# Kernel tuning notes

Measured on AMD Instinct MI355X. Metric: run time of the kernel, lower is better.

The kernel has to match this reference:

```python
import jax, jax.numpy as jnp
import numpy as np

S, B, D, F, E, K = 1024, 2, 512, 2048, 8, 2


def setup_inputs() -> dict:
    key = jax.random.key(0)
    ks = jax.random.split(key, 12)
    s = lambda *sh: 1.0 / np.sqrt(sh[0])
    inp = {
        "x": jax.random.normal(ks[0], (S, B, D), dtype=jnp.float32),
        # gate: nn.Linear(d_model, n_experts)
        "Wg": jax.random.normal(ks[1], (D, E), dtype=jnp.float32) * s(D),
        "bg": jnp.zeros((E,), dtype=jnp.float32),
        # routed experts: stacked FFN params (E copies of expert)
        "W1": jax.random.normal(ks[2], (E, D, F), dtype=jnp.float32) * s(D),
        "b1": jnp.zeros((E, F), dtype=jnp.float32),
        "W2": jax.random.normal(ks[3], (E, F, D), dtype=jnp.float32) * s(F),
        "b2": jnp.zeros((E, D), dtype=jnp.float32),
        # shared expert (single FFN)
        "Ws1": jax.random.normal(ks[4], (D, F), dtype=jnp.float32) * s(D),
        "bs1": jnp.zeros((F,), dtype=jnp.float32),
        "Ws2": jax.random.normal(ks[5], (F, D), dtype=jnp.float32) * s(F),
        "bs2": jnp.zeros((D,), dtype=jnp.float32),
    }
    return inp


def reference(x, Wg, bg, W1, b1, W2, b2, Ws1, bs1, Ws2, bs2):
    # gate_logits: (S, B, E)
    gate_logits = jnp.einsum("sbd,de->sbe", x, Wg) + bg
    # top-k per token (eval mode: k = n_experts_per_token, t = 1.0)
    weights, selected = jax.lax.top_k(gate_logits, K)  # (S,B,K)
    weights = jax.nn.softmax(weights.astype(jnp.float32), axis=-1)
    # combine weights per expert: (S,B,E)
    onehot = jax.nn.one_hot(selected, E, dtype=weights.dtype)  # (S,B,K,E)
    comb = jnp.einsum("sbk,sbke->sbe", weights, onehot)
    # routed experts computed densely, combined with per-token routing weight
    h = jax.nn.relu(jnp.einsum("sbd,edf->sbef", x, W1) + b1)  # (S,B,E,F)
    y = jnp.einsum("sbef,efd->sbed", h, W2) + b2              # (S,B,E,D)
    out = jnp.einsum("sbe,sbed->sbd", comb, y)
    # shared expert, scaled by 1/k
    hs = jax.nn.relu(jnp.einsum("sbd,df->sbf", x, Ws1) + bs1)
    shared = jnp.einsum("sbf,fd->sbd", hs, Ws2) + bs2
    out = out + (1.0 / K) * shared
    return out
```

## Files before the change

kernel.cpp:

```cpp
#include <hip/hip_runtime.h>
#include <hip/hip_bf16.h>
#include <stdint.h>

#define TT 2048
#define DD 512
#define FF 2048
#define EE 8

typedef unsigned short u16;
typedef __attribute__((ext_vector_type(8))) unsigned short ushort8v;
typedef __attribute__((ext_vector_type(8))) short short8;
typedef __attribute__((ext_vector_type(4))) float float4v;

__device__ __forceinline__ u16 f2bf(float f) {
    unsigned u = __float_as_uint(f);
    u += 0x7FFF + ((u >> 16) & 1);
    return (u16)(u >> 16);
}

__device__ __forceinline__ void gl_lds16(const u16* g, u16* l) {
    __builtin_amdgcn_global_load_lds(
        (const __attribute__((address_space(1))) unsigned int*)g,
        (__attribute__((address_space(3))) unsigned int*)l, 16, 0, 0);
}

#define WS_HB   0ull
#define WS_XG   (WS_HB + 6144ull*2048*2)
#define WS_WT1  (WS_XG + 2048ull*512*2)
#define WS_ME   (WS_WT1 + 9ull*2048*512*2)
#define WS_MW   (WS_ME + 16384)
#define WS_RT   (WS_MW + 16384)
#define WS_WROW (WS_RT + 16384)
#define WS_TROW (WS_WROW + 16384)
#define WS_RTG  (WS_TROW + 16384)
#define WS_WT2  (WS_RTG + 128)
#define WS_YB   (WS_WT2 + 9ull*2048*512*2)
#define YS      (6144ull*512)
#define WS_NEED (WS_YB + 2ull*6144*512*4)

__device__ __forceinline__ void conv_unit(int j, const float* __restrict__ srcE,
                                          const float* __restrict__ srcS,
                                          u16* __restrict__ dst,
                                          int R, int C, int shC, u16* Ls) {
    int mid = j >> 8, t2 = j & 255;
    int tr = t2 >> shC, tc = t2 & ((1 << shC) - 1);
    int r0 = tr * 64, c0 = tc * 64;
    const float* src = (mid < 8) ? srcE + (size_t)mid * R * C : srcS;
    u16* dstm = dst + (size_t)mid * R * C;
    int t = threadIdx.x;
#pragma unroll
    for (int i = 0; i < 4; ++i) {
        int rr = (t >> 4) + i * 16;
        int cc = (t & 15) * 4;
        float4v v = *(const float4v*)(src + (size_t)(r0 + rr) * C + c0 + cc);
#pragma unroll
        for (int jx = 0; jx < 4; ++jx) Ls[(cc + jx) * 72 + rr] = f2bf(v[jx]);
    }
    __syncthreads();
#pragma unroll
    for (int jj = 0; jj < 2; ++jj) {
        int slot = t + jj * 256;
        int cc = slot >> 3, r8 = (slot & 7) * 8;
        ushort8v o = *(const ushort8v*)&Ls[cc * 72 + r8];
        *(ushort8v*)(dstm + (size_t)(c0 + cc) * R + r0 + r8) = o;
    }
}

__device__ __forceinline__ void gate_wave(int t, int lane,
                                          const float* __restrict__ x,
                                          const float* __restrict__ Wg,
                                          const float* __restrict__ bg,
                                          int* __restrict__ metaE,
                                          float* __restrict__ metaW,
                                          u16* __restrict__ xg) {
    const float* xp = x + (size_t)t * DD + lane * 8;
    float4v x0 = *(const float4v*)xp;
    float4v x1 = *(const float4v*)(xp + 4);
    float xf[8] = {x0[0], x0[1], x0[2], x0[3], x1[0], x1[1], x1[2], x1[3]};
    float acc[EE] = {0.f, 0.f, 0.f, 0.f, 0.f, 0.f, 0.f, 0.f};
#pragma unroll
    for (int g = 0; g < 8; ++g) {
        const float* wp = Wg + (size_t)(lane * 8 + g) * EE;
        float4v w0 = *(const float4v*)wp;
        float4v w1 = *(const float4v*)(wp + 4);
        acc[0] += xf[g] * w0[0]; acc[1] += xf[g] * w0[1];
        acc[2] += xf[g] * w0[2]; acc[3] += xf[g] * w0[3];
        acc[4] += xf[g] * w1[0]; acc[5] += xf[g] * w1[1];
        acc[6] += xf[g] * w1[2]; acc[7] += xf[g] * w1[3];
    }
#pragma unroll
    for (int off = 1; off < 64; off <<= 1) {
#pragma unroll
        for (int e = 0; e < EE; ++e) acc[e] += __shfl_xor(acc[e], off, 64);
    }
    ushort8v xv;
#pragma unroll
    for (int jx = 0; jx < 4; ++jx) xv[jx] = f2bf(x0[jx]);
#pragma unroll
    for (int jx = 0; jx < 4; ++jx) xv[4 + jx] = f2bf(x1[jx]);
    *(ushort8v*)(xg + (size_t)t * DD + lane * 8) = xv;
    if (lane == 0) {
#pragma unroll
        for (int e = 0; e < EE; ++e) acc[e] += bg[e];
        int e0 = 0; float l0 = acc[0];
#pragma unroll
        for (int e = 1; e < EE; ++e) if (acc[e] > l0) { l0 = acc[e]; e0 = e; }
        int e1 = -1; float l1 = -3.4e38f;
#pragma unroll
        for (int e = 0; e < EE; ++e)
            if (e != e0 && acc[e] > l1) { l1 = acc[e]; e1 = e; }
        float ex = __expf(l1 - l0);
        float w0 = 1.f / (1.f + ex);
        metaE[2 * t] = e0; metaE[2 * t + 1] = e1;
        metaW[2 * t] = w0; metaW[2 * t + 1] = 1.f - w0;
    }
}

__global__ __launch_bounds__(256) void fused1_k(
    const float* __restrict__ x, const float* __restrict__ Wg,
    const float* __restrict__ bg,
    const float* __restrict__ W1, const float* __restrict__ Ws1,
    const float* __restrict__ W2, const float* __restrict__ Ws2,
    float* __restrict__ out, u16* __restrict__ xg,
    u16* __restrict__ Wt1, u16* __restrict__ Wt2,
    int* __restrict__ metaE, float* __restrict__ metaW, int nconv) {
    __shared__ __align__(16) u16 Ls[64 * 72];
    int b = blockIdx.x, tid = threadIdx.x;
    if (b < nconv) {
        if (b < 2304) conv_unit(b, W1, Ws1, Wt1, DD, FF, 5, Ls);
        else          conv_unit(b - 2304, W2, Ws2, Wt2, FF, DD, 3, Ls);
    } else if (b < nconv + 512) {
        int gb = b - nconv;
        gate_wave(gb * 4 + (tid >> 6), tid & 63, x, Wg, bg, metaE, metaW, xg);
    } else {
        int zb = b - nconv - 512;
        float* op = out + (size_t)zb * 8192;
#pragma unroll
        for (int it = 0; it < 8; ++it)
            *(float4v*)(op + it * 1024 + tid * 4) = (float4v){0.f, 0.f, 0.f, 0.f};
    }
}

__global__ __launch_bounds__(256) void conv2_k(const float* __restrict__ W2,
                                               const float* __restrict__ Ws2,
                                               u16* __restrict__ Wt2) {
    __shared__ __align__(16) u16 Ls[64 * 72];
    conv_unit(blockIdx.x, W2, Ws2, Wt2, FF, DD, 3, Ls);
}

__global__ __launch_bounds__(256) void rank_k(const int* __restrict__ metaE,
                                              const float* __restrict__ metaW,
                                              int* __restrict__ routing,
                                              int* __restrict__ rtok,
                                              float* __restrict__ wrow,
                                              int* __restrict__ trow) {
    __shared__ __align__(16) char smem[16384];
    u16* er      = (u16*)smem;
    int* segCnt  = (int*)(smem + 8192);
    int* segBase = (int*)(smem + 10240);
    int* expTot  = (int*)(smem + 12288);
    int tid = threadIdx.x, wv = tid >> 6, lane = tid & 63;
    unsigned long long below = (lane == 0) ? 0ull : ((~0ull) >> (64 - lane));
    for (int s = wv * 16; s < wv * 16 + 16; ++s) {
        int entry = s * 64 + lane;
        int e = metaE[entry];
        int rk = 0;
#pragma unroll
        for (int ee = 0; ee < 8; ++ee) {
            unsigned long long m = __ballot(e == ee);
            if (e == ee) rk = __popcll(m & below);
            if (lane == ee) segCnt[s * 8 + ee] = __popcll(m);
        }
        er[entry] = (u16)(e | (rk << 4));
    }
    __syncthreads();
    if (tid < 8) {
        int s = 0;
        for (int g = 0; g < 64; ++g) { segBase[g * 8 + tid] = s; s += segCnt[g * 8 + tid]; }
        expTot[tid] = s;
    }
    __syncthreads();
    if (tid == 0) {
        int s = 0;
        for (int e = 0; e < 8; ++e) { int c = expTot[e]; expTot[8 + e] = s; s += c; }
    }
    __syncthreads();
    if (tid < 8) { routing[tid] = expTot[8 + tid]; routing[8 + tid] = expTot[tid]; }
    for (int i = 0; i < 16; ++i) {
        int entry = tid + i * 256;
        int v = er[entry];
        int e = v & 15, rk = v >> 4;
        int row = expTot[8 + e] + segBase[(entry >> 6) * 8 + e] + rk;
        rtok[row] = entry >> 1;
        wrow[row] = metaW[entry];
        trow[entry] = row;
    }
}

__global__ __launch_bounds__(512) void gemmA_k(
    const u16* __restrict__ xg, const u16* __restrict__ Wt1,
    const float* __restrict__ b1, const float* __restrict__ bs1,
    const int* __restrict__ routing, const int* __restrict__ rtok,
    u16* __restrict__ hbuf) {
    __shared__ __align__(16) u16 SM[32768];
    u16* Asb[2] = {SM, SM + 8192};
    u16* Bsb[2] = {SM + 16384, SM + 24576};
    const int* offs = routing; const int* cnt = routing + 8;
    int j = blockIdx.x, tid = threadIdx.x;
    int rt, ct, Mloc, hRowBase, rowBase; bool routed;
    const u16* Bsrc; const float* bias;
    if (j < 256) {
        rt = j >> 4; ct = j & 15; Mloc = 128; rowBase = rt * 128;
        Bsrc = Wt1 + (size_t)8 * FF * DD; bias = bs1;
        hRowBase = 4096 + rt * 128; routed = false;
    } else {
        int jr = j - 256; int e = jr & 7; int rc = jr >> 3;
        rt = rc >> 4; ct = rc & 15;
        int M = cnt[e]; if (rt * 128 >= M) return;
        Mloc = M - rt * 128; if (Mloc > 128) Mloc = 128;
        rowBase = offs[e] + rt * 128;
        Bsrc = Wt1 + (size_t)e * FF * DD; bias = b1 + e * FF;
        hRowBase = rowBase; routed = true;
    }
    int n0 = ct * 128;
    int lane = tid & 63, w = tid >> 6, ln = lane & 15, quad = lane >> 4;
    int wm = w >> 2, wn = w & 3;
    int lr8 = lane >> 3;
    int cs = (lane & 7) ^ lr8;
    const u16* ApS[2];
#pragma unroll
    for (int i = 0; i < 2; ++i) {
        int r = w * 16 + i * 8 + lr8;
        int tok;
        if (routed) { int br = rowBase + r; if (br > 4095) br = 4095; tok = rtok[br]; }
        else tok = rowBase + r;
        ApS[i] = xg + (size_t)tok * DD + cs * 8;
    }
    const u16* BpS[2];
#pragma unroll
    for (int i = 0; i < 2; ++i) {
        int r = w * 16 + i * 8 + lr8;
        BpS[i] = Bsrc + (size_t)(n0 + r) * DD + cs * 8;
    }
    float4v acc[4][2];
#pragma unroll
    for (int a = 0; a < 4; ++a)
#pragma unroll
        for (int b = 0; b < 2; ++b) acc[a][b] = (float4v){0.f, 0.f, 0.f, 0.f};

    auto stage = [&](int kt, int pb) {
#pragma unroll
        for (int i = 0; i < 2; ++i)
            gl_lds16(ApS[i] + kt * 64, Asb[pb] + (w * 16 + i * 8) * 64);
#pragma unroll
        for (int i = 0; i < 2; ++i)
            gl_lds16(BpS[i] + kt * 64, Bsb[pb] + (w * 16 + i * 8) * 64);
    };

    stage(0, 0);
#pragma unroll
    for (int kt = 0; kt < 8; ++kt) {
        int pb = kt & 1;
        if (kt < 7) {
            stage(kt + 1, pb ^ 1);
            asm volatile("s_waitcnt vmcnt(4)" ::: "memory");
        } else {
            asm volatile("s_waitcnt vmcnt(0)" ::: "memory");
        }
        __builtin_amdgcn_s_barrier();
        __builtin_amdgcn_sched_barrier(0);
        const u16* Ab = Asb[pb]; const u16* Bb = Bsb[pb];
#pragma unroll
        for (int s = 0; s < 2; ++s) {
            int chs = ((s * 4 + quad) ^ (ln & 7)) * 8;
            short8 Af[4], Bf[2];
#pragma unroll
            for (int a = 0; a < 4; ++a) {
                int ra = wm * 64 + a * 16 + ln;
                Af[a] = *(const short8*)(Ab + ra * 64 + chs);
            }
#pragma unroll
            for (int b = 0; b < 2; ++b) {
                int rb = wn * 32 + b * 16 + ln;
                Bf[b] = *(const short8*)(Bb + rb * 64 + chs);
            }
#pragma unroll
            for (int a = 0; a < 4; ++a)
#pragma unroll
                for (int b = 0; b < 2; ++b)
                    acc[a][b] = __builtin_amdgcn_mfma_f32_16x16x32_bf16(Af[a], Bf[b], acc[a][b], 0, 0, 0);
        }
        __builtin_amdgcn_sched_barrier(0);
        __builtin_amdgcn_s_barrier();
    }
    __syncthreads();
    u16* Cs = SM;
#pragma unroll
    for (int b = 0; b < 2; ++b) {
        int n = wn * 32 + b * 16 + ln;
        float bv = bias[n0 + n];
#pragma unroll
        for (int a = 0; a < 4; ++a) {
#pragma unroll
            for (int i = 0; i < 4; ++i) {
                int lr = wm * 64 + a * 16 + quad * 4 + i;
                float v = acc[a][b][i] + bv;
                v = v > 0.f ? v : 0.f;
                Cs[lr * 136 + n] = f2bf(v);
            }
        }
    }
    __syncthreads();
#pragma unroll
    for (int p = 0; p < 4; ++p) {
        int idx = p * 512 + tid;
        int row = idx >> 4, ch = idx & 15;
        if (row < Mloc) {
            ushort8v o = *(const ushort8v*)(Cs + row * 136 + ch * 8);
            *(ushort8v*)(hbuf + (size_t)(hRowBase + row) * FF + n0 + ch * 8) = o;
        }
    }
}

__global__ __launch_bounds__(512) void gemmB_k(
    const u16* __restrict__ hbuf, const u16* __restrict__ Wt2,
    const float* __restrict__ b2, const float* __restrict__ bs2,
    const int* __restrict__ routing, float* __restrict__ ybuf) {
    __shared__ __align__(16) u16 As[2][128 * 64];
    __shared__ __align__(16) u16 Bs[2][128 * 64];
    const int* offs = routing; const int* cnt = routing + 8;
    int j = blockIdx.x, tid = threadIdx.x;
    int rt, ct, ks, Mloc, aRowBase;
    const u16* Bsrc; const float* bias;
    if (j < 128) {
        ks = j & 1; ct = (j >> 1) & 3; rt = j >> 3;
        Mloc = 128; aRowBase = 4096 + rt * 128;
        Bsrc = Wt2 + (size_t)8 * DD * FF; bias = bs2;
    } else {
        int jr = j - 128; int e = jr & 7; int rc = jr >> 3;
        ks = rc & 1; ct = (rc >> 1) & 3; rt = rc >> 3;
        int M = cnt[e]; if (rt * 128 >= M) return;
        Mloc = M - rt * 128; if (Mloc > 128) Mloc = 128;
        aRowBase = offs[e] + rt * 128;
        Bsrc = Wt2 + (size_t)e * DD * FF; bias = b2 + e * DD;
    }
    int n0 = ct * 128;
    int lane = tid & 63, w = tid >> 6, ln = lane & 15, quad = lane >> 4;
    int wm = w >> 2, wn = w & 3;
    int lr8 = lane >> 3;
    int cs = (lane & 7) ^ lr8;
    const u16* ApS[2];
#pragma unroll
    for (int i = 0; i < 2; ++i) {
        int r = w * 16 + i * 8 + lr8;
        ApS[i] = hbuf + (size_t)(aRowBase + r) * FF + ks * 1024 + cs * 8;
    }
    const u16* BpS[2];
#pragma unroll
    for (int i = 0; i < 2; ++i) {
        int r = w * 16 + i * 8 + lr8;
        BpS[i] = Bsrc + (size_t)(n0 + r) * FF + ks * 1024 + cs * 8;
    }
    float4v acc[4][2];
#pragma unroll
    for (int a = 0; a < 4; ++a)
#pragma unroll
        for (int b = 0; b < 2; ++b) acc[a][b] = (float4v){0.f, 0.f, 0.f, 0.f};

    auto stage = [&](int kt, int pb) {
#pragma unroll
        for (int i = 0; i < 2; ++i)
            gl_lds16(ApS[i] + kt * 64, &As[pb][0] + (w * 16 + i * 8) * 64);
#pragma unroll
        for (int i = 0; i < 2; ++i)
            gl_lds16(BpS[i] + kt * 64, &Bs[pb][0] + (w * 16 + i * 8) * 64);
    };

    stage(0, 0);
#pragma unroll
    for (int kt = 0; kt < 16; ++kt) {
        int pb = kt & 1;
        if (kt < 15) {
            stage(kt + 1, pb ^ 1);
            asm volatile("s_waitcnt vmcnt(4)" ::: "memory");
        } else {
            asm volatile("s_waitcnt vmcnt(0)" ::: "memory");
        }
        __builtin_amdgcn_s_barrier();
        __builtin_amdgcn_sched_barrier(0);
        const u16* Ab = &As[pb][0]; const u16* Bb = &Bs[pb][0];
#pragma unroll
        for (int s = 0; s < 2; ++s) {
            int chs = ((s * 4 + quad) ^ (ln & 7)) * 8;
            short8 Af[4], Bf[2];
#pragma unroll
            for (int a = 0; a < 4; ++a) {
                int ra = wm * 64 + a * 16 + ln;
                Af[a] = *(const short8*)(Ab + ra * 64 + chs);
            }
#pragma unroll
            for (int b = 0; b < 2; ++b) {
                int rb = wn * 32 + b * 16 + ln;
                Bf[b] = *(const short8*)(Bb + rb * 64 + chs);
            }
#pragma unroll
            for (int a = 0; a < 4; ++a)
#pragma unroll
                for (int b = 0; b < 2; ++b)
                    acc[a][b] = __builtin_amdgcn_mfma_f32_16x16x32_bf16(Af[a], Bf[b], acc[a][b], 0, 0, 0);
        }
        __builtin_amdgcn_sched_barrier(0);
        __builtin_amdgcn_s_barrier();
    }
    float* yb = ybuf + (size_t)ks * YS;
#pragma unroll
    for (int b = 0; b < 2; ++b) {
        int n = n0 + wn * 32 + b * 16 + ln;
        float bv = (ks == 0) ? bias[n] : 0.f;
#pragma unroll
        for (int a = 0; a < 4; ++a) {
#pragma unroll
            for (int i = 0; i < 4; ++i) {
                int lr = wm * 64 + a * 16 + quad * 4 + i;
                if (lr < Mloc)
                    yb[(size_t)(aRowBase + lr) * DD + n] = acc[a][b][i] + bv;
            }
        }
    }
}

__global__ __launch_bounds__(256) void combine_k(
    const float* __restrict__ ybuf, const int* __restrict__ trow,
    const float* __restrict__ metaW, float* __restrict__ out) {
    int tid = threadIdx.x;
    int tok = blockIdx.x * 2 + (tid >> 7);
    int q = (tid & 127) * 4;
    int r0 = trow[2 * tok], r1 = trow[2 * tok + 1];
    float w0 = metaW[2 * tok], w1 = metaW[2 * tok + 1];
    const float* ya = ybuf;
    const float* yb = ybuf + YS;
    float4v y0a = *(const float4v*)(ya + (size_t)r0 * DD + q);
    float4v y0b = *(const float4v*)(yb + (size_t)r0 * DD + q);
    float4v y1a = *(const float4v*)(ya + (size_t)r1 * DD + q);
    float4v y1b = *(const float4v*)(yb + (size_t)r1 * DD + q);
    float4v ysa = *(const float4v*)(ya + (size_t)(4096 + tok) * DD + q);
    float4v ysb = *(const float4v*)(yb + (size_t)(4096 + tok) * DD + q);
    float4v o;
#pragma unroll
    for (int i = 0; i < 4; ++i)
        o[i] = w0 * (y0a[i] + y0b[i]) + w1 * (y1a[i] + y1b[i]) + 0.5f * (ysa[i] + ysb[i]);
    *(float4v*)(out + (size_t)tok * DD + q) = o;
}

__global__ __launch_bounds__(256) void gemmBat_k(
    const u16* __restrict__ hbuf, const u16* __restrict__ Wt2,
    const float* __restrict__ b2, const float* __restrict__ bs2,
    const int* __restrict__ routing, const int* __restrict__ rtok,
    const float* __restrict__ wrow, float* __restrict__ out) {
    __shared__ __align__(16) u16 As[2][64 * 64];
    __shared__ __align__(16) u16 Bs[2][128 * 64];
    const int* offs = routing; const int* cnt = routing + 8;
    int j = blockIdx.x, tid = threadIdx.x;
    int rt, ct, ks, Mloc, aRowBase; bool sh;
    const u16* Bsrc; const float* bias;
    if (j < 256) {
        sh = true; rt = j >> 3; int sub = j & 7; ct = sub >> 1; ks = sub & 1;
        Mloc = 64; aRowBase = 4096 + rt * 64;
        Bsrc = Wt2 + (size_t)8 * DD * FF; bias = bs2;
    } else {
        sh = false; int jr = j - 256; int e = jr & 7; int rc = jr >> 3;
        rt = rc >> 3; ct = (rc >> 1) & 3; ks = rc & 1;
        int M = cnt[e]; if (rt * 64 >= M) return;
        Mloc = M - rt * 64; if (Mloc > 64) Mloc = 64;
        aRowBase = offs[e] + rt * 64;
        Bsrc = Wt2 + (size_t)e * DD * FF; bias = b2 + e * DD;
    }
    int n0 = ct * 128;
    int lane = tid & 63, w = tid >> 6, ln = lane & 15, quad = lane >> 4;
    int lr8 = lane >> 3;
    int cs = (lane & 7) ^ lr8;
    const u16* ApS[2];
#pragma unroll
    for (int i = 0; i < 2; ++i) {
        int r = w * 16 + i * 8 + lr8;
        ApS[i] = hbuf + (size_t)(aRowBase + r) * FF + ks * 1024 + cs * 8;
    }
    const u16* BpS[4];
#pragma unroll
    for (int i = 0; i < 4; ++i) {
        int r = w * 32 + i * 8 + lr8;
        BpS[i] = Bsrc + (size_t)(n0 + r) * FF + ks * 1024 + cs * 8;
    }
    float4v acc[2][4];
#pragma unroll
    for (int a = 0; a < 2; ++a)
#pragma unroll
        for (int b = 0; b < 4; ++b) acc[a][b] = (float4v){0.f, 0.f, 0.f, 0.f};
    auto stage = [&](int kt, int pb) {
        u16* Ab = &As[pb][0]; u16* Bb = &Bs[pb][0];
#pragma unroll
        for (int i = 0; i < 2; ++i)
            gl_lds16(ApS[i] + kt * 64, Ab + (w * 16 + i * 8) * 64);
#pragma unroll
        for (int i = 0; i < 4; ++i)
            gl_lds16(BpS[i] + kt * 64, Bb + (w * 32 + i * 8) * 64);
    };
    stage(0, 0);
#pragma unroll
    for (int kt = 0; kt < 16; ++kt) {
        int pb = kt & 1;
        if (kt < 15) {
            stage(kt + 1, pb ^ 1);
            asm volatile("s_waitcnt vmcnt(6)" ::: "memory");
        } else {
            asm volatile("s_waitcnt vmcnt(0)" ::: "memory");
        }
        __builtin_amdgcn_s_barrier();
        __builtin_amdgcn_sched_barrier(0);
        const u16* Ab = &As[pb][0]; const u16* Bb = &Bs[pb][0];
#pragma unroll
        for (int s = 0; s < 2; ++s) {
            int chs = ((s * 4 + quad) ^ (ln & 7)) * 8;
            short8 Af[2], Bf[4];
#pragma unroll
            for (int a = 0; a < 2; ++a) {
                int ra = (w & 1) * 32 + a * 16 + ln;
                Af[a] = *(const short8*)(Ab + ra * 64 + chs);
            }
#pragma unroll
            for (int b = 0; b < 4; ++b) {
                int rb = (w >> 1) * 64 + b * 16 + ln;
                Bf[b] = *(const short8*)(Bb + rb * 64 + chs);
            }
#pragma unroll
            for (int a = 0; a < 2; ++a)
#pragma unroll
                for (int b = 0; b < 4; ++b)
                    acc[a][b] = __builtin_amdgcn_mfma_f32_16x16x32_bf16(Af[a], Bf[b], acc[a][b], 0, 0, 0);
        }
        __builtin_amdgcn_sched_barrier(0);
        __builtin_amdgcn_s_barrier();
    }
    float bv[4];
#pragma unroll
    for (int b = 0; b < 4; ++b)
        bv[b] = (ks == 0) ? bias[n0 + (w >> 1) * 64 + b * 16 + ln] : 0.f;
#pragma unroll
    for (int a = 0; a < 2; ++a) {
#pragma unroll
        for (int i = 0; i < 4; ++i) {
            int lr = (w & 1) * 32 + a * 16 + quad * 4 + i;
            if (lr < Mloc) {
                int row = aRowBase + lr;
                int t; float wr;
                if (sh) { t = row - 4096; wr = 0.5f; }
                else    { t = rtok[row]; wr = wrow[row]; }
                float* op = out + (size_t)t * DD;
#pragma unroll
                for (int b = 0; b < 4; ++b) {
                    int n = n0 + (w >> 1) * 64 + b * 16 + ln;
                    atomicAdd(op + n, wr * (acc[a][b][i] + bv[b]));
                }
            }
        }
    }
}

extern "C" void kernel_launch(void* const* d_in, const int* in_sizes, int n_in,
                              void* d_out, int out_size, void* d_ws, size_t ws_size,
                              hipStream_t stream) {
    const float* x   = (const float*)d_in[0];
    const float* Wg  = (const float*)d_in[1];
    const float* bg  = (const float*)d_in[2];
    const float* W1  = (const float*)d_in[3];
    const float* b1  = (const float*)d_in[4];
    const float* W2  = (const float*)d_in[5];
    const float* b2  = (const float*)d_in[6];
    const float* Ws1 = (const float*)d_in[7];
    const float* bs1 = (const float*)d_in[8];
    const float* Ws2 = (const float*)d_in[9];
    const float* bs2 = (const float*)d_in[10];
    float* out = (float*)d_out;

    char* ws = (char*)d_ws;
    u16*   hbuf    = (u16*)(ws + WS_HB);
    u16*   xg      = (u16*)(ws + WS_XG);
    u16*   Wt1     = (u16*)(ws + WS_WT1);
    int*   metaE   = (int*)(ws + WS_ME);
    float* metaW   = (float*)(ws + WS_MW);
    int*   rtok    = (int*)(ws + WS_RT);
    float* wrow    = (float*)(ws + WS_WROW);
    int*   trow    = (int*)(ws + WS_TROW);
    int*   routing = (int*)(ws + WS_RTG);
    bool   big     = ws_size >= WS_NEED;
    u16*   Wt2     = big ? (u16*)(ws + WS_WT2) : Wt1;
    float* ybuf    = (float*)(ws + WS_YB);
    int    nconv   = big ? 4608 : 2304;
    int    ngrid1  = big ? (nconv + 512) : (nconv + 640);

    fused1_k<<<ngrid1, 256, 0, stream>>>(x, Wg, bg, W1, Ws1, W2, Ws2,
                                         out, xg, Wt1, Wt2, metaE, metaW, nconv);
    rank_k<<<1, 256, 0, stream>>>(metaE, metaW, routing, rtok, wrow, trow);
    gemmA_k<<<4352, 512, 0, stream>>>(xg, Wt1, b1, bs1, routing, rtok, hbuf);
    if (big) {
        gemmB_k<<<2176, 512, 0, stream>>>(hbuf, Wt2, b2, bs2, routing, ybuf);
        combine_k<<<1024, 256, 0, stream>>>(ybuf, trow, metaW, out);
    } else {
        conv2_k<<<2304, 256, 0, stream>>>(W2, Ws2, Wt2);
        gemmBat_k<<<4352, 256, 0, stream>>>(hbuf, Wt2, b2, bs2, routing, rtok, wrow, out);
    }
}
```

Baseline: 196.8 us.

## Drop split-K in second expert GEMM and swizzle LDS in weight conversion

```diff
diff --git a/kernel.cpp b/kernel.cpp
--- a/kernel.cpp
+++ b/kernel.cpp
@@ -54,14 +54,19 @@
         int cc = (t & 15) * 4;
         float4v v = *(const float4v*)(src + (size_t)(r0 + rr) * C + c0 + cc);
 #pragma unroll
-        for (int jx = 0; jx < 4; ++jx) Ls[(cc + jx) * 72 + rr] = f2bf(v[jx]);
+        for (int jx = 0; jx < 4; ++jx) {
+            int c = cc + jx;
+            int rs = rr ^ (((c >> 2) & 3) << 4);
+            Ls[c * 72 + rs] = f2bf(v[jx]);
+        }
     }
     __syncthreads();
 #pragma unroll
     for (int jj = 0; jj < 2; ++jj) {
         int slot = t + jj * 256;
         int cc = slot >> 3, r8 = (slot & 7) * 8;
-        ushort8v o = *(const ushort8v*)&Ls[cc * 72 + r8];
+        int r8s = r8 ^ (((cc >> 2) & 3) << 4);
+        ushort8v o = *(const ushort8v*)&Ls[cc * 72 + r8s];
         *(ushort8v*)(dstm + (size_t)(c0 + cc) * R + r0 + r8) = o;
     }
 }
@@ -330,15 +335,15 @@
     __shared__ __align__(16) u16 Bs[2][128 * 64];
     const int* offs = routing; const int* cnt = routing + 8;
     int j = blockIdx.x, tid = threadIdx.x;
-    int rt, ct, ks, Mloc, aRowBase;
+    int rt, ct, Mloc, aRowBase;
     const u16* Bsrc; const float* bias;
-    if (j < 128) {
-        ks = j & 1; ct = (j >> 1) & 3; rt = j >> 3;
+    if (j < 64) {
+        rt = j >> 2; ct = j & 3;
         Mloc = 128; aRowBase = 4096 + rt * 128;
         Bsrc = Wt2 + (size_t)8 * DD * FF; bias = bs2;
     } else {
-        int jr = j - 128; int e = jr & 7; int rc = jr >> 3;
-        ks = rc & 1; ct = (rc >> 1) & 3; rt = rc >> 3;
+        int jr = j - 64; int e = jr & 7; int rc = jr >> 3;
+        ct = rc & 3; rt = rc >> 2;
         int M = cnt[e]; if (rt * 128 >= M) return;
         Mloc = M - rt * 128; if (Mloc > 128) Mloc = 128;
         aRowBase = offs[e] + rt * 128;
@@ -353,13 +358,13 @@
 #pragma unroll
     for (int i = 0; i < 2; ++i) {
         int r = w * 16 + i * 8 + lr8;
-        ApS[i] = hbuf + (size_t)(aRowBase + r) * FF + ks * 1024 + cs * 8;
+        ApS[i] = hbuf + (size_t)(aRowBase + r) * FF + cs * 8;
     }
     const u16* BpS[2];
 #pragma unroll
     for (int i = 0; i < 2; ++i) {
         int r = w * 16 + i * 8 + lr8;
-        BpS[i] = Bsrc + (size_t)(n0 + r) * FF + ks * 1024 + cs * 8;
+        BpS[i] = Bsrc + (size_t)(n0 + r) * FF + cs * 8;
     }
     float4v acc[4][2];
 #pragma unroll
@@ -378,9 +383,9 @@
 
     stage(0, 0);
 #pragma unroll
-    for (int kt = 0; kt < 16; ++kt) {
+    for (int kt = 0; kt < 32; ++kt) {
         int pb = kt & 1;
-        if (kt < 15) {
+        if (kt < 31) {
             stage(kt + 1, pb ^ 1);
             asm volatile("s_waitcnt vmcnt(4)" ::: "memory");
         } else {
@@ -412,18 +417,17 @@
         __builtin_amdgcn_sched_barrier(0);
         __builtin_amdgcn_s_barrier();
     }
-    float* yb = ybuf + (size_t)ks * YS;
 #pragma unroll
     for (int b = 0; b < 2; ++b) {
         int n = n0 + wn * 32 + b * 16 + ln;
-        float bv = (ks == 0) ? bias[n] : 0.f;
+        float bv = bias[n];
 #pragma unroll
         for (int a = 0; a < 4; ++a) {
 #pragma unroll
             for (int i = 0; i < 4; ++i) {
                 int lr = wm * 64 + a * 16 + quad * 4 + i;
                 if (lr < Mloc)
-                    yb[(size_t)(aRowBase + lr) * DD + n] = acc[a][b][i] + bv;
+                    ybuf[(size_t)(aRowBase + lr) * DD + n] = acc[a][b][i] + bv;
             }
         }
     }
@@ -437,18 +441,12 @@
     int q = (tid & 127) * 4;
     int r0 = trow[2 * tok], r1 = trow[2 * tok + 1];
     float w0 = metaW[2 * tok], w1 = metaW[2 * tok + 1];
-    const float* ya = ybuf;
-    const float* yb = ybuf + YS;
-    float4v y0a = *(const float4v*)(ya + (size_t)r0 * DD + q);
-    float4v y0b = *(const float4v*)(yb + (size_t)r0 * DD + q);
-    float4v y1a = *(const float4v*)(ya + (size_t)r1 * DD + q);
-    float4v y1b = *(const float4v*)(yb + (size_t)r1 * DD + q);
-    float4v ysa = *(const float4v*)(ya + (size_t)(4096 + tok) * DD + q);
-    float4v ysb = *(const float4v*)(yb + (size_t)(4096 + tok) * DD + q);
+    float4v y0 = *(const float4v*)(ybuf + (size_t)r0 * DD + q);
+    float4v y1 = *(const float4v*)(ybuf + (size_t)r1 * DD + q);
+    float4v ys = *(const float4v*)(ybuf + (size_t)(4096 + tok) * DD + q);
     float4v o;
 #pragma unroll
-    for (int i = 0; i < 4; ++i)
-        o[i] = w0 * (y0a[i] + y0b[i]) + w1 * (y1a[i] + y1b[i]) + 0.5f * (ysa[i] + ysb[i]);
+    for (int i = 0; i < 4; ++i) o[i] = w0 * y0[i] + w1 * y1[i] + 0.5f * ys[i];
     *(float4v*)(out + (size_t)tok * DD + q) = o;
 }
 
@@ -603,7 +601,7 @@
     rank_k<<<1, 256, 0, stream>>>(metaE, metaW, routing, rtok, wrow, trow);
     gemmA_k<<<4352, 512, 0, stream>>>(xg, Wt1, b1, bs1, routing, rtok, hbuf);
     if (big) {
-        gemmB_k<<<2176, 512, 0, stream>>>(hbuf, Wt2, b2, bs2, routing, ybuf);
+        gemmB_k<<<1088, 512, 0, stream>>>(hbuf, Wt2, b2, bs2, routing, ybuf);
         combine_k<<<1024, 256, 0, stream>>>(ybuf, trow, metaW, out);
     } else {
         conv2_k<<<2304, 256, 0, stream>>>(W2, Ws2, Wt2);
```

New measurement: 203.9 us. +3.6%, slower.
